# Optimization experiments

Hardware: AMD Instinct MI355X
Metric: run time of the kernel (lower is better)

Reference implementation:

```python
import jax, jax.numpy as jnp
import numpy as np

NB_STEPS = 50  # Clenshaw-Curtis quadrature with NB_STEPS+1 points
B = 16384


def _cc_weights(nb_steps):
    # Faithful port of UMNN compute_cc_weights (ParallelNeuralIntegral)
    lam = np.arange(nb_steps + 1, dtype=np.float64).reshape(-1, 1)
    lam = np.cos((lam @ lam.T) * np.pi / nb_steps)
    lam[:, 0] *= 0.5
    lam[:, -1] *= 0.5
    lam = lam * 2.0 / nb_steps
    k = np.arange(nb_steps + 1, dtype=np.float64).reshape(-1, 1)
    den = 1.0 - k ** 2
    den[0] = 1.0
    den[np.arange(1, nb_steps + 1, 2)] = 1.0  # avoid div-by-zero; zeroed below
    W = 2.0 / den
    W[0] = 1.0
    W[np.arange(1, nb_steps + 1, 2)] = 0.0
    cc_w = (lam.T @ W).astype(np.float32)  # [S, 1]
    steps = np.cos(np.arange(nb_steps + 1).reshape(-1, 1) * np.pi / nb_steps).astype(np.float32)  # [S, 1]
    return jnp.asarray(cc_w), jnp.asarray(steps)


def _integrand(xh, w1, b1, w2, b2, w3, b3, w4, b4):
    # IntegrandNN: Linear+ReLU x3, Linear+ELU, then +1 (guarantees positivity-ish)
    a = jax.nn.relu(xh @ w1 + b1)
    a = jax.nn.relu(a @ w2 + b2)
    a = jax.nn.relu(a @ w3 + b3)
    a = jax.nn.elu(a @ w4 + b4)
    return a + 1.0


def setup_inputs() -> dict:
    key = jax.random.key(0)
    ks = jax.random.split(key, 10)
    s = 0.1  # small weight scale for numerical sanity
    return {
        "x": jax.random.normal(ks[0], (B, 1), dtype=jnp.float32),
        "h": jax.random.normal(ks[1], (B, 1), dtype=jnp.float32),
        "w1": jax.random.normal(ks[2], (2, 128), dtype=jnp.float32) * s,
        "b1": jax.random.normal(ks[3], (128,), dtype=jnp.float32) * s,
        "w2": jax.random.normal(ks[4], (128, 128), dtype=jnp.float32) * s,
        "b2": jax.random.normal(ks[5], (128,), dtype=jnp.float32) * s,
        "w3": jax.random.normal(ks[6], (128, 128), dtype=jnp.float32) * s,
        "b3": jax.random.normal(ks[7], (128,), dtype=jnp.float32) * s,
        "w4": jax.random.normal(ks[8], (128, 1), dtype=jnp.float32) * s,
        "b4": jax.random.normal(ks[9], (1,), dtype=jnp.float32) * s,
    }


def reference(x, h, w1, b1, w2, b2, w3, b3, w4, b4):
    cc_w, steps = _cc_weights(NB_STEPS)  # [S,1], [S,1]
    S = NB_STEPS + 1
    x0 = jnp.zeros_like(x)
    xT = x  # x0 + nb_steps * (x - x0) / nb_steps
    # quadrature abscissae mapped to [x0, xT]: [B, S, 1]
    X = x0[:, None, :] + (xT - x0)[:, None, :] * (steps[None, :, :] + 1.0) * 0.5
    hh = jnp.broadcast_to(h[:, None, :], (x.shape[0], S, h.shape[1]))
    xh = jnp.concatenate([X, hh], axis=-1).reshape(x.shape[0] * S, -1)  # [B*S, in_d]
    dz = _integrand(xh, w1, b1, w2, b2, w3, b3, w4, b4).reshape(x.shape[0], S, -1)
    z = jnp.sum(dz * cc_w[None, :, :], axis=1) * (xT - x0) * 0.5  # [B, out_d]
    # MonotonicNN.forward: integral + offset (offset = h); self.net(h) output is discarded
    return z + h
```

## Files before the change

kernel.cpp:

```cpp
#include <hip/hip_runtime.h>
#include <hip/hip_bf16.h>

#define NSTEP 50
#define S51 51
#define HID 128
#define MT 64
#define BPB 16
#define RPB (BPB * S51)
#define NTILE 13
#define GRID (16384 / BPB)
#define BLOCK 256

typedef __attribute__((ext_vector_type(4))) float floatx4;
typedef __attribute__((ext_vector_type(16))) float floatx16;
typedef __attribute__((ext_vector_type(8))) __bf16 bf16x8;

__device__ __forceinline__ unsigned pk4_fp8(float v0, float v1, float v2, float v3) {
    unsigned r = (unsigned)__builtin_amdgcn_cvt_pk_fp8_f32(v0, v1, 0, false);
    r = (unsigned)__builtin_amdgcn_cvt_pk_fp8_f32(v2, v3, (int)r, true);
    return r;
}

__device__ __forceinline__ int sw8(int row, int chunk) {
    return row * HID + ((chunk ^ (row & 15)) << 3);
}

__device__ __forceinline__ floatx16 ld_bias16(const float* bs, int base) {
    const floatx4 t0 = *(const floatx4*)(&bs[base]);
    const floatx4 t1 = *(const floatx4*)(&bs[base + 8]);
    const floatx4 t2 = *(const floatx4*)(&bs[base + 16]);
    const floatx4 t3 = *(const floatx4*)(&bs[base + 24]);
    floatx16 v = {t0[0], t0[1], t0[2], t0[3], t1[0], t1[1], t1[2], t1[3],
                  t2[0], t2[1], t2[2], t2[3], t3[0], t3[1], t3[2], t3[3]};
    return v;
}

__device__ __forceinline__ void l1_tile(unsigned char* dst, int t,
                                        const float* tsp, const float* b1s,
                                        bf16x8 aw, float xv, __bf16 hb, float hm,
                                        int l31, int hi, int mi) {
    const int s1 = 4 * t + (l31 >> 4);
    bf16x8 bx0 = {}, bx1 = {};
    bx0[0] = (__bf16)(xv * tsp[s1] * hm);     bx0[1] = hb;
    bx1[0] = (__bf16)(xv * tsp[s1 + 2] * hm); bx1[1] = hb;
    const floatx16 ci = ld_bias16(b1s, mi * 32 + 4 * hi);
    floatx16 d0 = __builtin_amdgcn_mfma_f32_32x32x16_bf16(aw, bx0, ci, 0, 0, 0);
    floatx16 d1 = __builtin_amdgcn_mfma_f32_32x32x16_bf16(aw, bx1, ci, 0, 0, 0);
#pragma unroll
    for (int g = 0; g < 4; ++g) {
        const int chI = mi * 4 + g;
        unsigned p0 = pk4_fp8(fmaxf(d0[4 * g + 0], 0.0f), fmaxf(d0[4 * g + 1], 0.0f),
                              fmaxf(d0[4 * g + 2], 0.0f), fmaxf(d0[4 * g + 3], 0.0f));
        *(unsigned*)(&dst[sw8(l31, chI) + 4 * hi]) = p0;
        unsigned p1 = pk4_fp8(fmaxf(d1[4 * g + 0], 0.0f), fmaxf(d1[4 * g + 1], 0.0f),
                              fmaxf(d1[4 * g + 2], 0.0f), fmaxf(d1[4 * g + 3], 0.0f));
        *(unsigned*)(&dst[sw8(l31 + 32, chI) + 4 * hi]) = p1;
    }
}

__launch_bounds__(BLOCK, 4)
__global__ void monotonic_fused(const float* __restrict__ x, const float* __restrict__ h,
                                const float* __restrict__ w1, const float* __restrict__ b1,
                                const float* __restrict__ w2, const float* __restrict__ b2,
                                const float* __restrict__ w3, const float* __restrict__ b3,
                                const float* __restrict__ w4, const float* __restrict__ b4,
                                float* __restrict__ out) {
    __shared__ __align__(16) unsigned char A1[2][MT * HID];
    __shared__ __align__(16) unsigned char A2[2][MT * HID];
    __shared__ float b1s[HID], b2s[HID], b3s[HID], w4s[HID];
    __shared__ float fs[S51], ts[52];
    __shared__ float xs[BPB], hs[BPB];
    __shared__ float posum[2][4][MT];

    const int tid = threadIdx.x;
    const int lane = tid & 63;
    const int mi = tid >> 6;
    const int l31 = lane & 31;
    const int hi = lane >> 5;

    if (tid < HID) {
        b1s[tid] = b1[tid]; b2s[tid] = b2[tid]; b3s[tid] = b3[tid]; w4s[tid] = w4[tid];
    }
    if (tid < BPB) {
        xs[tid] = x[blockIdx.x * BPB + tid];
        hs[tid] = h[blockIdx.x * BPB + tid];
    }
    if (tid < 52) {
        if (tid < S51) {
            const float PI50 = 0.06283185307179586f;
            float acc = 1.0f;
            for (int i = 2; i <= 50; i += 2) {
                int m = (i * tid) % 100;
                acc += (2.0f / (1.0f - (float)(i * i))) * cosf((float)m * PI50);
            }
            float ccw = acc * 0.04f * ((tid == 0 || tid == NSTEP) ? 0.5f : 1.0f);
            fs[tid] = ccw * 0.5f;
            ts[tid] = (cosf((float)tid * PI50) + 1.0f) * 0.5f;
        } else {
            ts[51] = 0.0f;
        }
    }
    const float b4v = b4[0];
    const float hm = (hi == 0) ? 1.0f : 0.0f;

    long w2f[8], w3f[8];
    {
        const int irow = mi * 32 + l31;
#pragma unroll
        for (int kc = 0; kc < 8; ++kc) {
            const int kb = kc * 16 + hi * 8;
            unsigned lo2 = pk4_fp8(w2[(kb + 0) * HID + irow], w2[(kb + 1) * HID + irow],
                                   w2[(kb + 2) * HID + irow], w2[(kb + 3) * HID + irow]);
            unsigned hi2 = pk4_fp8(w2[(kb + 4) * HID + irow], w2[(kb + 5) * HID + irow],
                                   w2[(kb + 6) * HID + irow], w2[(kb + 7) * HID + irow]);
            w2f[kc] = (long)(((unsigned long long)hi2 << 32) | lo2);
            unsigned lo3 = pk4_fp8(w3[(kb + 0) * HID + irow], w3[(kb + 1) * HID + irow],
                                   w3[(kb + 2) * HID + irow], w3[(kb + 3) * HID + irow]);
            unsigned hi3 = pk4_fp8(w3[(kb + 4) * HID + irow], w3[(kb + 5) * HID + irow],
                                   w3[(kb + 6) * HID + irow], w3[(kb + 7) * HID + irow]);
            w3f[kc] = (long)(((unsigned long long)hi3 << 32) | lo3);
        }
    }
    bf16x8 aw = {};
    {
        const int j = mi * 32 + l31;
        aw[0] = (__bf16)(w1[j] * hm);
        aw[1] = (__bf16)(w1[HID + j] * hm);
    }
    __syncthreads();

    const float xv = xs[l31 & 15];
    const __bf16 hb = (__bf16)(hs[l31 & 15] * hm);
    float accq = 0.0f;

    l1_tile(A1[0], 0, ts, b1s, aw, xv, hb, hm, l31, hi, mi);
    __syncthreads();

    for (int s = 0; s <= NTILE; ++s) {
        const int pa = s & 1, pb = pa ^ 1;
        floatx16 a0, a1, c0, c1;

        if (s < NTILE) {
            const floatx16 ci = ld_bias16(b2s, mi * 32 + 4 * hi);
            long f0 = *(const long*)(&A1[pa][sw8(l31, hi)]);
            long f1 = *(const long*)(&A1[pa][sw8(l31 + 32, hi)]);
            a0 = __builtin_amdgcn_mfma_f32_32x32x16_fp8_fp8(w2f[0], f0, ci, 0, 0, 0);
            a1 = __builtin_amdgcn_mfma_f32_32x32x16_fp8_fp8(w2f[0], f1, ci, 0, 0, 0);
#pragma unroll
            for (int kc = 1; kc < 8; ++kc) {
                f0 = *(const long*)(&A1[pa][sw8(l31, kc * 2 + hi)]);
                f1 = *(const long*)(&A1[pa][sw8(l31 + 32, kc * 2 + hi)]);
                a0 = __builtin_amdgcn_mfma_f32_32x32x16_fp8_fp8(w2f[kc], f0, a0, 0, 0, 0);
                a1 = __builtin_amdgcn_mfma_f32_32x32x16_fp8_fp8(w2f[kc], f1, a1, 0, 0, 0);
            }
        }
        if (s >= 1) {
            const floatx16 ci = ld_bias16(b3s, mi * 32 + 4 * hi);
            long g0 = *(const long*)(&A2[pb][sw8(l31, hi)]);
            long g1 = *(const long*)(&A2[pb][sw8(l31 + 32, hi)]);
            c0 = __builtin_amdgcn_mfma_f32_32x32x16_fp8_fp8(w3f[0], g0, ci, 0, 0, 0);
            c1 = __builtin_amdgcn_mfma_f32_32x32x16_fp8_fp8(w3f[0], g1, ci, 0, 0, 0);
#pragma unroll
            for (int kc = 1; kc < 8; ++kc) {
                g0 = *(const long*)(&A2[pb][sw8(l31, kc * 2 + hi)]);
                g1 = *(const long*)(&A2[pb][sw8(l31 + 32, kc * 2 + hi)]);
                c0 = __builtin_amdgcn_mfma_f32_32x32x16_fp8_fp8(w3f[kc], g0, c0, 0, 0, 0);
                c1 = __builtin_amdgcn_mfma_f32_32x32x16_fp8_fp8(w3f[kc], g1, c1, 0, 0, 0);
            }
        }
        if (s >= 2 && tid < MT) {
            int lr = (s - 2) * MT + tid;
            if (lr < RPB) {
                float u = posum[pa][0][tid] + posum[pa][1][tid] + posum[pa][2][tid]
                        + posum[pa][3][tid] + b4v;
                float dz = u > 0.0f ? u + 1.0f : __expf(u);
                accq += dz * fs[lr >> 4];
            }
        }
        if (s < NTILE) {
#pragma unroll
            for (int g = 0; g < 4; ++g) {
                const int chI = mi * 4 + g;
                unsigned p0 = pk4_fp8(fmaxf(a0[4 * g + 0], 0.0f), fmaxf(a0[4 * g + 1], 0.0f),
                                      fmaxf(a0[4 * g + 2], 0.0f), fmaxf(a0[4 * g + 3], 0.0f));
                *(unsigned*)(&A2[pa][sw8(l31, chI) + 4 * hi]) = p0;
                unsigned p1 = pk4_fp8(fmaxf(a1[4 * g + 0], 0.0f), fmaxf(a1[4 * g + 1], 0.0f),
                                      fmaxf(a1[4 * g + 2], 0.0f), fmaxf(a1[4 * g + 3], 0.0f));
                *(unsigned*)(&A2[pa][sw8(l31 + 32, chI) + 4 * hi]) = p1;
            }
        }
        if (s >= 1) {
            float p0 = 0.0f, p1 = 0.0f;
#pragma unroll
            for (int g = 0; g < 4; ++g) {
                const floatx4 w4v = *(const floatx4*)(&w4s[mi * 32 + 8 * g + 4 * hi]);
#pragma unroll
                for (int rr = 0; rr < 4; ++rr) {
                    p0 = fmaf(fmaxf(c0[4 * g + rr], 0.0f), w4v[rr], p0);
                    p1 = fmaf(fmaxf(c1[4 * g + rr], 0.0f), w4v[rr], p1);
                }
            }
            p0 += __shfl_xor(p0, 32);
            p1 += __shfl_xor(p1, 32);
            if (hi == 0) {
                posum[pb][mi][l31] = p0;
                posum[pb][mi][l31 + 32] = p1;
            }
        }
        if (s + 1 < NTILE) {
            l1_tile(A1[pb], s + 1, ts, b1s, aw, xv, hb, hm, l31, hi, mi);
        }
        __syncthreads();
    }

    if (tid < MT) {
        int lr = (NTILE - 1) * MT + tid;
        if (lr < RPB) {
            const int pf = (NTILE - 1) & 1;
            float u = posum[pf][0][tid] + posum[pf][1][tid] + posum[pf][2][tid]
                    + posum[pf][3][tid] + b4v;
            float dz = u > 0.0f ? u + 1.0f : __expf(u);
            accq += dz * fs[lr >> 4];
        }
        accq += __shfl_xor(accq, 16);
        accq += __shfl_xor(accq, 32);
        if (tid < BPB) out[blockIdx.x * BPB + tid] = hs[tid] + accq * xs[tid];
    }
}

extern "C" void kernel_launch(void* const* d_in, const int* in_sizes, int n_in,
                              void* d_out, int out_size, void* d_ws, size_t ws_size,
                              hipStream_t stream) {
    const float* x  = (const float*)d_in[0];
    const float* h  = (const float*)d_in[1];
    const float* w1 = (const float*)d_in[2];
    const float* b1 = (const float*)d_in[3];
    const float* w2 = (const float*)d_in[4];
    const float* b2 = (const float*)d_in[5];
    const float* w3 = (const float*)d_in[6];
    const float* b3 = (const float*)d_in[7];
    const float* w4 = (const float*)d_in[8];
    const float* b4 = (const float*)d_in[9];
    float* out = (float*)d_out;

    monotonic_fused<<<GRID, BLOCK, 0, stream>>>(x, h, w1, b1, w2, b2, w3, b3, w4, b4, out);
}
```

Measured before the change: 136.5 us.

## Deepen layer pipeline and interleave layer-2/3 MFMAs with precomputed swizzle offsets

Restructures the per-tile loop into a deeper software pipeline. The layer-3 accumulators now live across iterations, so the layer-4 reduction of tile t runs one iteration after its layer-3 MFMAs, and the final sum is folded into the loop. Layer-2 and layer-3 MFMA chains are interleaved in one k-loop to expose more independent MFMA work. Swizzled LDS addresses are precomputed once and stepped by XOR instead of recomputed through sw8. The cost is two extra loop iterations and more registers kept live, which may pressure occupancy under the 4-wave launch bounds.

```diff
diff --git a/kernel.cpp b/kernel.cpp
--- a/kernel.cpp
+++ b/kernel.cpp
@@ -21,9 +21,6 @@
     return r;
 }
 
-__device__ __forceinline__ int sw8(int row, int chunk) {
-    return row * HID + ((chunk ^ (row & 15)) << 3);
-}
 
 __device__ __forceinline__ floatx16 ld_bias16(const float* bs, int base) {
     const floatx4 t0 = *(const floatx4*)(&bs[base]);
@@ -38,7 +35,7 @@
 __device__ __forceinline__ void l1_tile(unsigned char* dst, int t,
                                         const float* tsp, const float* b1s,
                                         bf16x8 aw, float xv, __bf16 hb, float hm,
-                                        int l31, int hi, int mi) {
+                                        int wbm, int l31, int hi, int mi) {
     const int s1 = 4 * t + (l31 >> 4);
     bf16x8 bx0 = {}, bx1 = {};
     bx0[0] = (__bf16)(xv * tsp[s1] * hm);     bx0[1] = hb;
@@ -48,13 +45,12 @@
     floatx16 d1 = __builtin_amdgcn_mfma_f32_32x32x16_bf16(aw, bx1, ci, 0, 0, 0);
 #pragma unroll
     for (int g = 0; g < 4; ++g) {
-        const int chI = mi * 4 + g;
         unsigned p0 = pk4_fp8(fmaxf(d0[4 * g + 0], 0.0f), fmaxf(d0[4 * g + 1], 0.0f),
                               fmaxf(d0[4 * g + 2], 0.0f), fmaxf(d0[4 * g + 3], 0.0f));
-        *(unsigned*)(&dst[sw8(l31, chI) + 4 * hi]) = p0;
+        *(unsigned*)(&dst[wbm ^ (g << 3)]) = p0;
         unsigned p1 = pk4_fp8(fmaxf(d1[4 * g + 0], 0.0f), fmaxf(d1[4 * g + 1], 0.0f),
                               fmaxf(d1[4 * g + 2], 0.0f), fmaxf(d1[4 * g + 3], 0.0f));
-        *(unsigned*)(&dst[sw8(l31 + 32, chI) + 4 * hi]) = p1;
+        *(unsigned*)(&dst[(wbm ^ (g << 3)) + 4096]) = p1;
     }
 }
 
@@ -133,63 +129,20 @@
     const __bf16 hb = (__bf16)(hs[l31 & 15] * hm);
     float accq = 0.0f;
 
-    l1_tile(A1[0], 0, ts, b1s, aw, xv, hb, hm, l31, hi, mi);
+    const int rb  = l31 * HID + ((l31 & 15) << 3);
+    const int rbh = rb ^ (hi << 3);
+    const int wbm = (rb + 4 * hi) ^ (mi << 5);
+
+    l1_tile(A1[0], 0, ts, b1s, aw, xv, hb, hm, wbm, l31, hi, mi);
     __syncthreads();
 
-    for (int s = 0; s <= NTILE; ++s) {
+    floatx16 c0 = {}, c1 = {};
+
+    for (int s = 0; s <= NTILE + 2; ++s) {
         const int pa = s & 1, pb = pa ^ 1;
-        floatx16 a0, a1, c0, c1;
-
-        if (s < NTILE) {
-            const floatx16 ci = ld_bias16(b2s, mi * 32 + 4 * hi);
-            long f0 = *(const long*)(&A1[pa][sw8(l31, hi)]);
-            long f1 = *(const long*)(&A1[pa][sw8(l31 + 32, hi)]);
-            a0 = __builtin_amdgcn_mfma_f32_32x32x16_fp8_fp8(w2f[0], f0, ci, 0, 0, 0);
-            a1 = __builtin_amdgcn_mfma_f32_32x32x16_fp8_fp8(w2f[0], f1, ci, 0, 0, 0);
-#pragma unroll
-            for (int kc = 1; kc < 8; ++kc) {
-                f0 = *(const long*)(&A1[pa][sw8(l31, kc * 2 + hi)]);
-                f1 = *(const long*)(&A1[pa][sw8(l31 + 32, kc * 2 + hi)]);
-                a0 = __builtin_amdgcn_mfma_f32_32x32x16_fp8_fp8(w2f[kc], f0, a0, 0, 0, 0);
-                a1 = __builtin_amdgcn_mfma_f32_32x32x16_fp8_fp8(w2f[kc], f1, a1, 0, 0, 0);
-            }
-        }
-        if (s >= 1) {
-            const floatx16 ci = ld_bias16(b3s, mi * 32 + 4 * hi);
-            long g0 = *(const long*)(&A2[pb][sw8(l31, hi)]);
-            long g1 = *(const long*)(&A2[pb][sw8(l31 + 32, hi)]);
-            c0 = __builtin_amdgcn_mfma_f32_32x32x16_fp8_fp8(w3f[0], g0, ci, 0, 0, 0);
-            c1 = __builtin_amdgcn_mfma_f32_32x32x16_fp8_fp8(w3f[0], g1, ci, 0, 0, 0);
-#pragma unroll
-            for (int kc = 1; kc < 8; ++kc) {
-                g0 = *(const long*)(&A2[pb][sw8(l31, kc * 2 + hi)]);
-                g1 = *(const long*)(&A2[pb][sw8(l31 + 32, kc * 2 + hi)]);
-                c0 = __builtin_amdgcn_mfma_f32_32x32x16_fp8_fp8(w3f[kc], g0, c0, 0, 0, 0);
-                c1 = __builtin_amdgcn_mfma_f32_32x32x16_fp8_fp8(w3f[kc], g1, c1, 0, 0, 0);
-            }
-        }
-        if (s >= 2 && tid < MT) {
-            int lr = (s - 2) * MT + tid;
-            if (lr < RPB) {
-                float u = posum[pa][0][tid] + posum[pa][1][tid] + posum[pa][2][tid]
-                        + posum[pa][3][tid] + b4v;
-                float dz = u > 0.0f ? u + 1.0f : __expf(u);
-                accq += dz * fs[lr >> 4];
-            }
-        }
-        if (s < NTILE) {
-#pragma unroll
-            for (int g = 0; g < 4; ++g) {
-                const int chI = mi * 4 + g;
-                unsigned p0 = pk4_fp8(fmaxf(a0[4 * g + 0], 0.0f), fmaxf(a0[4 * g + 1], 0.0f),
-                                      fmaxf(a0[4 * g + 2], 0.0f), fmaxf(a0[4 * g + 3], 0.0f));
-                *(unsigned*)(&A2[pa][sw8(l31, chI) + 4 * hi]) = p0;
-                unsigned p1 = pk4_fp8(fmaxf(a1[4 * g + 0], 0.0f), fmaxf(a1[4 * g + 1], 0.0f),
-                                      fmaxf(a1[4 * g + 2], 0.0f), fmaxf(a1[4 * g + 3], 0.0f));
-                *(unsigned*)(&A2[pa][sw8(l31 + 32, chI) + 4 * hi]) = p1;
-            }
-        }
-        if (s >= 1) {
+        floatx16 a0, a1;
+
+        if (s >= 2 && s <= NTILE + 1) {
             float p0 = 0.0f, p1 = 0.0f;
 #pragma unroll
             for (int g = 0; g < 4; ++g) {
@@ -203,25 +156,86 @@
             p0 += __shfl_xor(p0, 32);
             p1 += __shfl_xor(p1, 32);
             if (hi == 0) {
-                posum[pb][mi][l31] = p0;
-                posum[pb][mi][l31 + 32] = p1;
+                posum[pa][mi][l31] = p0;
+                posum[pa][mi][l31 + 32] = p1;
+            }
+        }
+        if (s >= 3 && tid < MT) {
+            int lr = (s - 3) * MT + tid;
+            if (lr < RPB) {
+                float u = posum[pb][0][tid] + posum[pb][1][tid] + posum[pb][2][tid]
+                        + posum[pb][3][tid] + b4v;
+                float dz = u > 0.0f ? u + 1.0f : __expf(u);
+                accq += dz * fs[lr >> 4];
+            }
+        }
+        if (s >= 1 && s < NTILE) {
+            const floatx16 ci2 = ld_bias16(b2s, mi * 32 + 4 * hi);
+            const floatx16 ci3 = ld_bias16(b3s, mi * 32 + 4 * hi);
+            long f0 = *(const long*)(&A1[pa][rbh]);
+            long f1 = *(const long*)(&A1[pa][rbh + 4096]);
+            long g0 = *(const long*)(&A2[pb][rbh]);
+            long g1 = *(const long*)(&A2[pb][rbh + 4096]);
+            a0 = __builtin_amdgcn_mfma_f32_32x32x16_fp8_fp8(w2f[0], f0, ci2, 0, 0, 0);
+            a1 = __builtin_amdgcn_mfma_f32_32x32x16_fp8_fp8(w2f[0], f1, ci2, 0, 0, 0);
+            c0 = __builtin_amdgcn_mfma_f32_32x32x16_fp8_fp8(w3f[0], g0, ci3, 0, 0, 0);
+            c1 = __builtin_amdgcn_mfma_f32_32x32x16_fp8_fp8(w3f[0], g1, ci3, 0, 0, 0);
+#pragma unroll
+            for (int kc = 1; kc < 8; ++kc) {
+                f0 = *(const long*)(&A1[pa][rbh ^ (kc << 4)]);
+                f1 = *(const long*)(&A1[pa][(rbh ^ (kc << 4)) + 4096]);
+                g0 = *(const long*)(&A2[pb][rbh ^ (kc << 4)]);
+                g1 = *(const long*)(&A2[pb][(rbh ^ (kc << 4)) + 4096]);
+                a0 = __builtin_amdgcn_mfma_f32_32x32x16_fp8_fp8(w2f[kc], f0, a0, 0, 0, 0);
+                a1 = __builtin_amdgcn_mfma_f32_32x32x16_fp8_fp8(w2f[kc], f1, a1, 0, 0, 0);
+                c0 = __builtin_amdgcn_mfma_f32_32x32x16_fp8_fp8(w3f[kc], g0, c0, 0, 0, 0);
+                c1 = __builtin_amdgcn_mfma_f32_32x32x16_fp8_fp8(w3f[kc], g1, c1, 0, 0, 0);
+            }
+        } else if (s < NTILE) {
+            const floatx16 ci2 = ld_bias16(b2s, mi * 32 + 4 * hi);
+            long f0 = *(const long*)(&A1[pa][rbh]);
+            long f1 = *(const long*)(&A1[pa][rbh + 4096]);
+            a0 = __builtin_amdgcn_mfma_f32_32x32x16_fp8_fp8(w2f[0], f0, ci2, 0, 0, 0);
+            a1 = __builtin_amdgcn_mfma_f32_32x32x16_fp8_fp8(w2f[0], f1, ci2, 0, 0, 0);
+#pragma unroll
+            for (int kc = 1; kc < 8; ++kc) {
+                f0 = *(const long*)(&A1[pa][rbh ^ (kc << 4)]);
+                f1 = *(const long*)(&A1[pa][(rbh ^ (kc << 4)) + 4096]);
+                a0 = __builtin_amdgcn_mfma_f32_32x32x16_fp8_fp8(w2f[kc], f0, a0, 0, 0, 0);
+                a1 = __builtin_amdgcn_mfma_f32_32x32x16_fp8_fp8(w2f[kc], f1, a1, 0, 0, 0);
+            }
+        } else if (s <= NTILE) {
+            const floatx16 ci3 = ld_bias16(b3s, mi * 32 + 4 * hi);
+            long g0 = *(const long*)(&A2[pb][rbh]);
+            long g1 = *(const long*)(&A2[pb][rbh + 4096]);
+            c0 = __builtin_amdgcn_mfma_f32_32x32x16_fp8_fp8(w3f[0], g0, ci3, 0, 0, 0);
+            c1 = __builtin_amdgcn_mfma_f32_32x32x16_fp8_fp8(w3f[0], g1, ci3, 0, 0, 0);
+#pragma unroll
+            for (int kc = 1; kc < 8; ++kc) {
+                g0 = *(const long*)(&A2[pb][rbh ^ (kc << 4)]);
+                g1 = *(const long*)(&A2[pb][(rbh ^ (kc << 4)) + 4096]);
+                c0 = __builtin_amdgcn_mfma_f32_32x32x16_fp8_fp8(w3f[kc], g0, c0, 0, 0, 0);
+                c1 = __builtin_amdgcn_mfma_f32_32x32x16_fp8_fp8(w3f[kc], g1, c1, 0, 0, 0);
+            }
+        }
+        if (s < NTILE) {
+#pragma unroll
+            for (int g = 0; g < 4; ++g) {
+                unsigned p0 = pk4_fp8(fmaxf(a0[4 * g + 0], 0.0f), fmaxf(a0[4 * g + 1], 0.0f),
+                                      fmaxf(a0[4 * g + 2], 0.0f), fmaxf(a0[4 * g + 3], 0.0f));
+                *(unsigned*)(&A2[pa][wbm ^ (g << 3)]) = p0;
+                unsigned p1 = pk4_fp8(fmaxf(a1[4 * g + 0], 0.0f), fmaxf(a1[4 * g + 1], 0.0f),
+                                      fmaxf(a1[4 * g + 2], 0.0f), fmaxf(a1[4 * g + 3], 0.0f));
+                *(unsigned*)(&A2[pa][(wbm ^ (g << 3)) + 4096]) = p1;
             }
         }
         if (s + 1 < NTILE) {
-            l1_tile(A1[pb], s + 1, ts, b1s, aw, xv, hb, hm, l31, hi, mi);
+            l1_tile(A1[pb], s + 1, ts, b1s, aw, xv, hb, hm, wbm, l31, hi, mi);
         }
         __syncthreads();
     }
 
     if (tid < MT) {
-        int lr = (NTILE - 1) * MT + tid;
-        if (lr < RPB) {
-            const int pf = (NTILE - 1) & 1;
-            float u = posum[pf][0][tid] + posum[pf][1][tid] + posum[pf][2][tid]
-                    + posum[pf][3][tid] + b4v;
-            float dz = u > 0.0f ? u + 1.0f : __expf(u);
-            accq += dz * fs[lr >> 4];
-        }
         accq += __shfl_xor(accq, 16);
         accq += __shfl_xor(accq, 32);
         if (tid < BPB) out[blockIdx.x * BPB + tid] = hs[tid] + accq * xs[tid];
```

Result: slower. 179.4 us (+31.4%).
